# Performance work log

Hardware: AMD Instinct MI355X
Metric: run time of the kernel (lower is better)

The kernel has to match this reference:

```python
import jax, jax.numpy as jnp
import numpy as np
from jax import lax

WS = 7          # window size
SHIFT = WS // 2 # shift for odd blocks
NH = 4          # num heads
PATCH = 4


def _rel_index(ws):
    # standard Swin relative position index, shape (ws*ws, ws*ws)
    coords = np.stack(np.meshgrid(np.arange(ws), np.arange(ws), indexing='ij')).reshape(2, -1)
    rel = (coords[:, :, None] - coords[:, None, :]).transpose(1, 2, 0)
    rel[..., 0] += ws - 1
    rel[..., 1] += ws - 1
    rel[..., 0] *= 2 * ws - 1
    return jnp.asarray(rel.sum(-1))


def _attn_mask(H, W, ws, s):
    # BasicLayer mask for cyclic shift: (nW, ws*ws, ws*ws) with 0 / -100
    img = np.zeros((H, W))
    cnt = 0
    for hs in (slice(0, -ws), slice(-ws, -s), slice(-s, None)):
        for wsl in (slice(0, -ws), slice(-ws, -s), slice(-s, None)):
            img[hs, wsl] = cnt
            cnt += 1
    mw = img.reshape(H // ws, ws, W // ws, ws).transpose(0, 2, 1, 3).reshape(-1, ws * ws)
    diff = mw[:, None, :] - mw[:, :, None]
    return jnp.asarray(np.where(diff != 0, -100.0, 0.0).astype(np.float32))


def setup_inputs() -> dict:
    key = jax.random.key(0)
    ks = jax.random.split(key, 6)
    C = 128
    return {
        'x': jax.random.normal(ks[0], (16, 3, 448, 448), jnp.float32),
        'conv_w': jax.random.normal(ks[1], (C, 3, PATCH, PATCH), jnp.float32) * 0.02,
        'conv_b': jnp.zeros((C,), jnp.float32),
        'qkv_w': jax.random.normal(ks[2], (2, 3 * C, C), jnp.float32) * 0.02,
        'qkv_b': jnp.zeros((2, 3 * C), jnp.float32),
        'proj_w': jax.random.normal(ks[3], (2, C, C), jnp.float32) * 0.02,
        'proj_b': jnp.zeros((2, C), jnp.float32),
        'rpb': jax.random.normal(ks[4], (2, (2 * WS - 1) ** 2, NH), jnp.float32) * 0.02,
    }


def _forward(x, conv_w, conv_b, qkv_w, qkv_b, proj_w, proj_b, rpb):
    # patch embed: strided conv
    y = lax.conv_general_dilated(x, conv_w, (PATCH, PATCH), 'VALID',
                                 dimension_numbers=('NCHW', 'OIHW', 'NCHW'))
    y = y + conv_b[None, :, None, None]
    B, C, H, W = y.shape
    hd = C // NH
    scale = hd ** -0.5
    N = WS * WS
    nW = (H // WS) * (W // WS)
    t = y.reshape(B, C, H * W).transpose(0, 2, 1)  # (B, L, C)

    rel_idx = _rel_index(WS)                    # (N, N)
    mask = _attn_mask(H, W, WS, SHIFT)          # (nW, N, N)

    for i in range(2):
        shift = 0 if i % 2 == 0 else SHIFT
        xw = t.reshape(B, H, W, C)
        if shift > 0:
            xw = jnp.roll(xw, (-shift, -shift), axis=(1, 2))
        # window partition -> (B*nW, N, C)
        win = xw.reshape(B, H // WS, WS, W // WS, WS, C).transpose(0, 1, 3, 2, 4, 5).reshape(-1, N, C)
        qkv = win @ qkv_w[i].T + qkv_b[i]       # (B*nW, N, 3C)
        qkv = qkv.reshape(-1, N, 3, NH, hd).transpose(2, 0, 3, 1, 4)
        q, k, v = qkv[0], qkv[1], qkv[2]        # (B*nW, NH, N, hd)
        attn = jnp.einsum('wnid,wnjd->wnij', q * scale, k)
        bias = rpb[i][rel_idx].transpose(2, 0, 1)  # (NH, N, N)
        attn = attn + bias[None]
        if shift > 0:
            attn = (attn.reshape(B, nW, NH, N, N) + mask[None, :, None]).reshape(-1, NH, N, N)
        attn = jax.nn.softmax(attn, axis=-1)
        out = jnp.einsum('wnij,wnjd->wnid', attn, v).transpose(0, 2, 1, 3).reshape(-1, N, C)
        out = out @ proj_w[i].T + proj_b[i]
        # window reverse
        xw = out.reshape(B, H // WS, W // WS, WS, WS, C).transpose(0, 1, 3, 2, 4, 5).reshape(B, H, W, C)
        if shift > 0:
            xw = jnp.roll(xw, (shift, shift), axis=(1, 2))
        t = xw.reshape(B, H * W, C)

    return t.reshape(B, H, W, C).transpose(0, 3, 1, 2)  # (B, C, H, W)


def reference(x, conv_w, conv_b, qkv_w, qkv_b, proj_w, proj_b, rpb):
    return _forward(x, conv_w, conv_b, qkv_w, qkv_b, proj_w, proj_b, rpb)
```

## Files before the change

kernel.cpp:

```cpp
#include <hip/hip_runtime.h>

#define BB 16
#define CC 128
#define HH 112
#define NHH 4
#define WSZ 7
#define NN 49
#define SH 3

typedef _Float16 h8 __attribute__((ext_vector_type(8)));
typedef _Float16 h4 __attribute__((ext_vector_type(4)));
typedef float f4 __attribute__((ext_vector_type(4)));

__device__ __forceinline__ int rid3(int p) { return p < 105 ? 0 : (p < 109 ? 1 : 2); }

#define OFF_WIN 0
#define OFF_K   8704
#define OFF_Q   18944
#define OFF_VT  29184
#define OFF_P   0
#define OFF_O   18944

__global__ __launch_bounds__(256) void conv_embed(const float* __restrict__ x,
    const float* __restrict__ cw, const float* __restrict__ cb, _Float16* __restrict__ t0) {
  __shared__ float xs[3][4][448];
  __shared__ float wT[48][128];
  __shared__ float cbs[128];
  int bid = blockIdx.x;
  int b = bid / HH, oh = bid % HH;
  int tid = threadIdx.x;
  for (int idx = tid; idx < 3 * 4 * 448; idx += 256) {
    int ch = idx / 1792;
    int r = (idx / 448) & 3;
    int col = idx % 448;
    xs[ch][r][col] = x[((b * 3 + ch) * 448 + (oh * 4 + r)) * 448 + col];
  }
  for (int idx = tid; idx < 6144; idx += 256) {
    int c = idx / 48, k = idx - c * 48;
    wT[k][c] = cw[idx];
  }
  if (tid < 128) cbs[tid] = cb[tid];
  __syncthreads();
  int c0 = (tid & 31) << 2;
  int gg = tid >> 5;
  for (int it = 0; it < 4; ++it) {
    int gw0 = it * 32 + gg * 4;
    if (gw0 >= HH) break;
    float acc[4][4] = {};
#pragma unroll
    for (int k = 0; k < 48; ++k) {
      int ch = k >> 4, r = (k >> 2) & 3, j = k & 3;
      float4 wv = *(const float4*)&wT[k][c0];
#pragma unroll
      for (int d = 0; d < 4; ++d) {
        float xv = xs[ch][r][(gw0 + d) * 4 + j];
        acc[d][0] = fmaf(xv, wv.x, acc[d][0]);
        acc[d][1] = fmaf(xv, wv.y, acc[d][1]);
        acc[d][2] = fmaf(xv, wv.z, acc[d][2]);
        acc[d][3] = fmaf(xv, wv.w, acc[d][3]);
      }
    }
    float4 bv = *(const float4*)&cbs[c0];
#pragma unroll
    for (int d = 0; d < 4; ++d) {
      int gw = gw0 + d;
      h4 o;
      o[0] = (_Float16)(acc[d][0] + bv.x); o[1] = (_Float16)(acc[d][1] + bv.y);
      o[2] = (_Float16)(acc[d][2] + bv.z); o[3] = (_Float16)(acc[d][3] + bv.w);
      *(h4*)&t0[((size_t)(b * HH + oh) * HH + gw) * CC + c0] = o;
    }
  }
}

__global__ void prep(const float* __restrict__ qw, const float* __restrict__ qb,
                     const float* __restrict__ pw, const float* __restrict__ rpb,
                     _Float16* __restrict__ qwh, float* __restrict__ qbs,
                     _Float16* __restrict__ pwh, float* __restrict__ biasT) {
  const float scale = 0.17677669529663687f;
  int tid0 = blockIdx.x * blockDim.x + threadIdx.x;
  int stride = gridDim.x * blockDim.x;
  for (int idx = tid0; idx < 2 * 384 * 128; idx += stride) {
    int n = (idx >> 7) % 384;
    float v = qw[idx];
    if (n < 128) v *= scale;
    qwh[idx] = (_Float16)v;
  }
  for (int idx = tid0; idx < 2 * 384; idx += stride) {
    int n = idx % 384;
    float v = qb[idx];
    if (n < 128) v *= scale;
    qbs[idx] = v;
  }
  for (int idx = tid0; idx < 2 * 128 * 128; idx += stride)
    pwh[idx] = (_Float16)pw[idx];
  for (int idx = tid0; idx < 2 * 4 * 4 * 4 * 64 * 4; idx += stride) {
    int r = idx & 3;
    int lane = (idx >> 2) & 63;
    int it = (idx >> 8) & 3;
    int jt = (idx >> 10) & 3;
    int hh = (idx >> 12) & 3;
    int ll = idx >> 14;
    int i = it * 16 + (lane & 15);
    int j = jt * 16 + ((lane >> 4) * 4) + r;
    float v = 0.f;
    if (i < NN && j < NN) {
      int rel = ((i / 7 - j / 7) + 6) * 13 + ((i % 7 - j % 7) + 6);
      v = rpb[(ll * 169 + rel) * NHH + hh];
    }
    biasT[idx] = v;
  }
}

__global__ __launch_bounds__(256, 2) void swin_layer(
    const _Float16* __restrict__ tin, _Float16* __restrict__ toutB, float* __restrict__ outN,
    const _Float16* __restrict__ qwh, const float* __restrict__ qbs,
    const _Float16* __restrict__ pwh, const float* __restrict__ pb,
    const float* __restrict__ biasT, int shift, int writeN) {
  __shared__ _Float16 sm[38400];

  int tid = threadIdx.x;
  int wid = blockIdx.x;
  int b = wid >> 8;
  int wh = (wid >> 4) & 15, ww = wid & 15;
  int w = tid >> 6, l = tid & 63;
  int li = l & 15, lg = l >> 4;

  for (int c = tid; c < 64 * 16; c += 256) {
    int n = c >> 4, k0 = (c & 15) * 8;
    h8 v = {0, 0, 0, 0, 0, 0, 0, 0};
    if (n < NN) {
      int gh = wh * WSZ + n / 7 + shift; if (gh >= HH) gh -= HH;
      int gw = ww * WSZ + n % 7 + shift; if (gw >= HH) gw -= HH;
      v = *(const h8*)(tin + ((size_t)(b * HH + gh) * HH + gw) * CC + k0);
    }
    *(h8*)&sm[OFF_WIN + n * 136 + k0] = v;
  }
  __syncthreads();

  {
    h8 bW[4][4];
#pragma unroll
    for (int nt = 0; nt < 4; ++nt)
#pragma unroll
      for (int ks = 0; ks < 4; ++ks)
        bW[nt][ks] = *(const h8*)&sm[OFF_WIN + (nt * 16 + li) * 136 + ks * 32 + lg * 8];
    for (int mi = 0; mi < 6; ++mi) {
      int mt = w * 6 + mi;
      const _Float16* arow = qwh + (size_t)(mt * 16 + li) * 128 + lg * 8;
      h8 aA[4];
#pragma unroll
      for (int ks = 0; ks < 4; ++ks) aA[ks] = *(const h8*)(arow + ks * 32);
      f4 acc[4] = {};
#pragma unroll
      for (int ks = 0; ks < 4; ++ks)
#pragma unroll
        for (int nt = 0; nt < 4; ++nt)
          acc[nt] = __builtin_amdgcn_mfma_f32_16x16x32_f16(aA[ks], bW[nt][ks], acc[nt], 0, 0, 0);
      int dbase = mt * 16 + lg * 4;
      float4 bb = *(const float4*)&qbs[dbase];
#pragma unroll
      for (int nt = 0; nt < 4; ++nt) {
        int i = nt * 16 + li;
        float v0 = acc[nt][0] + bb.x, v1 = acc[nt][1] + bb.y;
        float v2 = acc[nt][2] + bb.z, v3 = acc[nt][3] + bb.w;
        if (mt < 8) {
          int hq = dbase >> 5, dh = dbase & 31;
          h4 v = {(_Float16)v0, (_Float16)v1, (_Float16)v2, (_Float16)v3};
          *(h4*)&sm[OFF_Q + hq * 2560 + i * 40 + dh] = v;
        } else if (mt < 16) {
          int d = dbase - 128, hq = d >> 5, dh = d & 31;
          h4 v = {(_Float16)v0, (_Float16)v1, (_Float16)v2, (_Float16)v3};
          *(h4*)&sm[OFF_K + hq * 2560 + i * 40 + dh] = v;
        } else {
          int d = dbase - 256, hq = d >> 5, dh = d & 31;
          sm[OFF_VT + hq * 2304 + (dh + 0) * 72 + i] = (_Float16)v0;
          sm[OFF_VT + hq * 2304 + (dh + 1) * 72 + i] = (_Float16)v1;
          sm[OFF_VT + hq * 2304 + (dh + 2) * 72 + i] = (_Float16)v2;
          sm[OFF_VT + hq * 2304 + (dh + 3) * 72 + i] = (_Float16)v3;
        }
      }
    }
  }
  __syncthreads();

  float inv[4];
  {
    int h = w;
    h8 aK[4], bQ[4];
#pragma unroll
    for (int jt = 0; jt < 4; ++jt)
      aK[jt] = *(const h8*)&sm[OFF_K + h * 2560 + (jt * 16 + li) * 40 + lg * 8];
#pragma unroll
    for (int it = 0; it < 4; ++it)
      bQ[it] = *(const h8*)&sm[OFF_Q + h * 2560 + (it * 16 + li) * 40 + lg * 8];
    f4 s[4][4] = {};
#pragma unroll
    for (int jt = 0; jt < 4; ++jt)
#pragma unroll
      for (int it = 0; it < 4; ++it)
        s[jt][it] = __builtin_amdgcn_mfma_f32_16x16x32_f16(aK[jt], bQ[it], s[jt][it], 0, 0, 0);
    const float* bT = biasT + h * 4096;
#pragma unroll
    for (int jt = 0; jt < 4; ++jt)
#pragma unroll
      for (int it = 0; it < 4; ++it) {
        f4 bb = *(const f4*)&bT[(jt * 4 + it) * 256 + l * 4];
#pragma unroll
        for (int r = 0; r < 4; ++r) {
          int j = jt * 16 + lg * 4 + r;
          float v = s[jt][it][r] + bb[r];
          s[jt][it][r] = (j < NN) ? v : -1e30f;
        }
      }
    if (shift && (wh == 15 || ww == 15)) {
      int regi[4], regj[4][4];
#pragma unroll
      for (int it = 0; it < 4; ++it) {
        int i = it * 16 + li;
        regi[it] = rid3(wh * WSZ + i / 7) * 3 + rid3(ww * WSZ + i % 7);
      }
#pragma unroll
      for (int jt = 0; jt < 4; ++jt)
#pragma unroll
        for (int r = 0; r < 4; ++r) {
          int j = jt * 16 + lg * 4 + r;
          regj[jt][r] = rid3(wh * WSZ + j / 7) * 3 + rid3(ww * WSZ + j % 7);
        }
#pragma unroll
      for (int jt = 0; jt < 4; ++jt)
#pragma unroll
        for (int it = 0; it < 4; ++it)
#pragma unroll
          for (int r = 0; r < 4; ++r)
            if (regj[jt][r] != regi[it]) s[jt][it][r] -= 100.f;
    }
    __syncthreads();

#pragma unroll
    for (int it = 0; it < 4; ++it) {
      float mx = -1e30f;
#pragma unroll
      for (int jt = 0; jt < 4; ++jt)
#pragma unroll
        for (int r = 0; r < 4; ++r) mx = fmaxf(mx, s[jt][it][r]);
      mx = fmaxf(mx, __shfl_xor(mx, 16));
      mx = fmaxf(mx, __shfl_xor(mx, 32));
      float sum = 0.f;
#pragma unroll
      for (int jt = 0; jt < 4; ++jt)
#pragma unroll
        for (int r = 0; r < 4; ++r) {
          float e = __expf(s[jt][it][r] - mx);
          s[jt][it][r] = e;
          sum += e;
        }
      sum += __shfl_xor(sum, 16);
      sum += __shfl_xor(sum, 32);
      inv[it] = 1.f / sum;
    }
#pragma unroll
    for (int it = 0; it < 4; ++it)
#pragma unroll
      for (int jt = 0; jt < 4; ++jt) {
        int i = it * 16 + li, j0 = jt * 16 + lg * 4;
        h4 v = {(_Float16)s[jt][it][0], (_Float16)s[jt][it][1],
                (_Float16)s[jt][it][2], (_Float16)s[jt][it][3]};
        *(h4*)&sm[OFF_P + h * 4608 + i * 72 + j0] = v;
      }
  }

  {
    int h = w;
    h8 aV[2][2], bP[4][2];
#pragma unroll
    for (int mt = 0; mt < 2; ++mt)
#pragma unroll
      for (int ks = 0; ks < 2; ++ks)
        aV[mt][ks] = *(const h8*)&sm[OFF_VT + h * 2304 + (mt * 16 + li) * 72 + ks * 32 + lg * 8];
#pragma unroll
    for (int nt = 0; nt < 4; ++nt)
#pragma unroll
      for (int ks = 0; ks < 2; ++ks)
        bP[nt][ks] = *(const h8*)&sm[OFF_P + h * 4608 + (nt * 16 + li) * 72 + ks * 32 + lg * 8];
    f4 o[2][4] = {};
#pragma unroll
    for (int ks = 0; ks < 2; ++ks)
#pragma unroll
      for (int mt = 0; mt < 2; ++mt)
#pragma unroll
        for (int nt = 0; nt < 4; ++nt)
          o[mt][nt] = __builtin_amdgcn_mfma_f32_16x16x32_f16(aV[mt][ks], bP[nt][ks], o[mt][nt], 0, 0, 0);
#pragma unroll
    for (int mt = 0; mt < 2; ++mt)
#pragma unroll
      for (int nt = 0; nt < 4; ++nt) {
        int i = nt * 16 + li;
        int d = h * 32 + mt * 16 + lg * 4;
        float is = inv[nt];
        h4 v = {(_Float16)(o[mt][nt][0] * is), (_Float16)(o[mt][nt][1] * is),
                (_Float16)(o[mt][nt][2] * is), (_Float16)(o[mt][nt][3] * is)};
        *(h4*)&sm[OFF_O + i * 136 + d] = v;
      }
  }
  __syncthreads();

  {
    h8 bO[4][4];
#pragma unroll
    for (int nt = 0; nt < 4; ++nt)
#pragma unroll
      for (int ks = 0; ks < 4; ++ks)
        bO[nt][ks] = *(const h8*)&sm[OFF_O + (nt * 16 + li) * 136 + ks * 32 + lg * 8];
    for (int mi = 0; mi < 2; ++mi) {
      int mt = w * 2 + mi;
      const _Float16* arow = pwh + (size_t)(mt * 16 + li) * 128 + lg * 8;
      h8 aP[4];
#pragma unroll
      for (int ks = 0; ks < 4; ++ks) aP[ks] = *(const h8*)(arow + ks * 32);
      f4 acc[4] = {};
#pragma unroll
      for (int ks = 0; ks < 4; ++ks)
#pragma unroll
        for (int nt = 0; nt < 4; ++nt)
          acc[nt] = __builtin_amdgcn_mfma_f32_16x16x32_f16(aP[ks], bO[nt][ks], acc[nt], 0, 0, 0);
      int dbase = mt * 16 + lg * 4;
      float4 bb = *(const float4*)&pb[dbase];
#pragma unroll
      for (int nt = 0; nt < 4; ++nt) {
        int i = nt * 16 + li;
        if (i < NN) {
          int gh = wh * WSZ + i / 7 + shift; if (gh >= HH) gh -= HH;
          int gw = ww * WSZ + i % 7 + shift; if (gw >= HH) gw -= HH;
          float v0 = acc[nt][0] + bb.x, v1 = acc[nt][1] + bb.y;
          float v2 = acc[nt][2] + bb.z, v3 = acc[nt][3] + bb.w;
          if (!writeN) {
            h4 v = {(_Float16)v0, (_Float16)v1, (_Float16)v2, (_Float16)v3};
            *(h4*)&toutB[((size_t)(b * HH + gh) * HH + gw) * CC + dbase] = v;
          } else {
            size_t base = ((size_t)(b * CC + dbase) * HH + gh) * HH + gw;
            outN[base] = v0;
            outN[base + (size_t)HH * HH] = v1;
            outN[base + (size_t)2 * HH * HH] = v2;
            outN[base + (size_t)3 * HH * HH] = v3;
          }
        }
      }
    }
  }
}

extern "C" void kernel_launch(void* const* d_in, const int* in_sizes, int n_in,
                              void* d_out, int out_size, void* d_ws, size_t ws_size,
                              hipStream_t stream) {
  const float* x = (const float*)d_in[0];
  const float* cw = (const float*)d_in[1];
  const float* cb = (const float*)d_in[2];
  const float* qkvw = (const float*)d_in[3];
  const float* qkvb = (const float*)d_in[4];
  const float* projw = (const float*)d_in[5];
  const float* projb = (const float*)d_in[6];
  const float* rpb = (const float*)d_in[7];
  float* out = (float*)d_out;

  char* ws = (char*)d_ws;
  _Float16* t0 = (_Float16*)ws;
  size_t off = (size_t)BB * HH * HH * CC * 2;
  _Float16* qwh = (_Float16*)(ws + off);  off += 2 * 384 * 128 * 2;
  _Float16* pwh = (_Float16*)(ws + off);  off += 2 * 128 * 128 * 2;
  float* qbs = (float*)(ws + off);        off += 2 * 384 * 4;
  float* biasT = (float*)(ws + off);

  prep<<<224, 256, 0, stream>>>(qkvw, qkvb, projw, rpb, qwh, qbs, pwh, biasT);
  conv_embed<<<BB * HH, 256, 0, stream>>>(x, cw, cb, t0);

  swin_layer<<<4096, 256, 0, stream>>>(t0, t0, nullptr,
      qwh, qbs, pwh, projb, biasT, 0, 0);
  swin_layer<<<4096, 256, 0, stream>>>(t0, nullptr, out,
      qwh + 384 * 128, qbs + 384, pwh + 128 * 128, projb + 128,
      biasT + 16384, SH, 1);
}
```

Before: 317.1 us.

## Cut swin_layer LDS with swizzled layouts and direct-global window loads

Window tokens for the QKV GEMM are now loaded straight from global memory into registers instead of being staged in LDS. Q/K/V/P/O tiles use an XOR-swizzled unpadded layout, which shrinks LDS from about 77KB to 49KB and allows occupancy to rise from 2 to 3 blocks per CU. Unshifted fp16 outputs are staged through LDS so the global write is coalesced 16-byte rows. In exchange there are extra barriers, a larger accumulator register footprint that may pressure the occupancy target, and redundant global reads of the QKV weights inside the k-loop.

```diff
diff --git a/kernel.cpp b/kernel.cpp
--- a/kernel.cpp
+++ b/kernel.cpp
@@ -14,12 +14,14 @@
 
 __device__ __forceinline__ int rid3(int p) { return p < 105 ? 0 : (p < 109 ? 1 : 2); }
 
-#define OFF_WIN 0
-#define OFF_K   8704
-#define OFF_Q   18944
-#define OFF_VT  29184
-#define OFF_P   0
-#define OFF_O   18944
+#define SWZ(row, j, CH) ((row) * ((CH) * 8) + (((((j) >> 3) ^ (row)) & ((CH) - 1)) << 3) + ((j) & 7))
+
+#define KB 0
+#define QB 8192
+#define VB 16384
+#define PB 0
+#define OB 16384
+#define YB 0
 
 __global__ __launch_bounds__(256) void conv_embed(const float* __restrict__ x,
     const float* __restrict__ cw, const float* __restrict__ cb, _Float16* __restrict__ t0) {
@@ -111,12 +113,12 @@
   }
 }
 
-__global__ __launch_bounds__(256, 2) void swin_layer(
+__global__ __launch_bounds__(256, 3) void swin_layer(
     const _Float16* __restrict__ tin, _Float16* __restrict__ toutB, float* __restrict__ outN,
     const _Float16* __restrict__ qwh, const float* __restrict__ qbs,
     const _Float16* __restrict__ pwh, const float* __restrict__ pb,
     const float* __restrict__ biasT, int shift, int writeN) {
-  __shared__ _Float16 sm[38400];
+  __shared__ _Float16 sm[24576];
 
   int tid = threadIdx.x;
   int wid = blockIdx.x;
@@ -125,58 +127,56 @@
   int w = tid >> 6, l = tid & 63;
   int li = l & 15, lg = l >> 4;
 
-  for (int c = tid; c < 64 * 16; c += 256) {
-    int n = c >> 4, k0 = (c & 15) * 8;
-    h8 v = {0, 0, 0, 0, 0, 0, 0, 0};
-    if (n < NN) {
-      int gh = wh * WSZ + n / 7 + shift; if (gh >= HH) gh -= HH;
-      int gw = ww * WSZ + n % 7 + shift; if (gw >= HH) gw -= HH;
-      v = *(const h8*)(tin + ((size_t)(b * HH + gh) * HH + gw) * CC + k0);
-    }
-    *(h8*)&sm[OFF_WIN + n * 136 + k0] = v;
-  }
-  __syncthreads();
+  const _Float16* tokp[4];
+#pragma unroll
+  for (int nt = 0; nt < 4; ++nt) {
+    int n = nt * 16 + li;
+    int gh = wh * WSZ + n / 7 + shift; if (gh >= HH) gh -= HH;
+    int gw = ww * WSZ + n % 7 + shift; if (gw >= HH) gw -= HH;
+    tokp[nt] = tin + ((size_t)(b * HH + gh) * HH + gw) * CC;
+  }
 
   {
-    h8 bW[4][4];
-#pragma unroll
-    for (int nt = 0; nt < 4; ++nt)
-#pragma unroll
-      for (int ks = 0; ks < 4; ++ks)
-        bW[nt][ks] = *(const h8*)&sm[OFF_WIN + (nt * 16 + li) * 136 + ks * 32 + lg * 8];
+    f4 acc[6][4] = {};
+#pragma unroll
+    for (int ks = 0; ks < 4; ++ks) {
+      h8 bW[4];
+#pragma unroll
+      for (int nt = 0; nt < 4; ++nt)
+        bW[nt] = *(const h8*)(tokp[nt] + ks * 32 + lg * 8);
+#pragma unroll
+      for (int mi = 0; mi < 6; ++mi) {
+        int mt = w * 6 + mi;
+        h8 a = *(const h8*)(qwh + (size_t)(mt * 16 + li) * 128 + ks * 32 + lg * 8);
+#pragma unroll
+        for (int nt = 0; nt < 4; ++nt)
+          acc[mi][nt] = __builtin_amdgcn_mfma_f32_16x16x32_f16(a, bW[nt], acc[mi][nt], 0, 0, 0);
+      }
+    }
+#pragma unroll
     for (int mi = 0; mi < 6; ++mi) {
       int mt = w * 6 + mi;
-      const _Float16* arow = qwh + (size_t)(mt * 16 + li) * 128 + lg * 8;
-      h8 aA[4];
-#pragma unroll
-      for (int ks = 0; ks < 4; ++ks) aA[ks] = *(const h8*)(arow + ks * 32);
-      f4 acc[4] = {};
-#pragma unroll
-      for (int ks = 0; ks < 4; ++ks)
-#pragma unroll
-        for (int nt = 0; nt < 4; ++nt)
-          acc[nt] = __builtin_amdgcn_mfma_f32_16x16x32_f16(aA[ks], bW[nt][ks], acc[nt], 0, 0, 0);
       int dbase = mt * 16 + lg * 4;
       float4 bb = *(const float4*)&qbs[dbase];
 #pragma unroll
       for (int nt = 0; nt < 4; ++nt) {
         int i = nt * 16 + li;
-        float v0 = acc[nt][0] + bb.x, v1 = acc[nt][1] + bb.y;
-        float v2 = acc[nt][2] + bb.z, v3 = acc[nt][3] + bb.w;
+        float v0 = acc[mi][nt][0] + bb.x, v1 = acc[mi][nt][1] + bb.y;
+        float v2 = acc[mi][nt][2] + bb.z, v3 = acc[mi][nt][3] + bb.w;
         if (mt < 8) {
           int hq = dbase >> 5, dh = dbase & 31;
           h4 v = {(_Float16)v0, (_Float16)v1, (_Float16)v2, (_Float16)v3};
-          *(h4*)&sm[OFF_Q + hq * 2560 + i * 40 + dh] = v;
+          *(h4*)&sm[QB + hq * 2048 + SWZ(i, dh, 4)] = v;
         } else if (mt < 16) {
           int d = dbase - 128, hq = d >> 5, dh = d & 31;
           h4 v = {(_Float16)v0, (_Float16)v1, (_Float16)v2, (_Float16)v3};
-          *(h4*)&sm[OFF_K + hq * 2560 + i * 40 + dh] = v;
+          *(h4*)&sm[KB + hq * 2048 + SWZ(i, dh, 4)] = v;
         } else {
           int d = dbase - 256, hq = d >> 5, dh = d & 31;
-          sm[OFF_VT + hq * 2304 + (dh + 0) * 72 + i] = (_Float16)v0;
-          sm[OFF_VT + hq * 2304 + (dh + 1) * 72 + i] = (_Float16)v1;
-          sm[OFF_VT + hq * 2304 + (dh + 2) * 72 + i] = (_Float16)v2;
-          sm[OFF_VT + hq * 2304 + (dh + 3) * 72 + i] = (_Float16)v3;
+          sm[VB + hq * 2048 + SWZ(dh + 0, i, 8)] = (_Float16)v0;
+          sm[VB + hq * 2048 + SWZ(dh + 1, i, 8)] = (_Float16)v1;
+          sm[VB + hq * 2048 + SWZ(dh + 2, i, 8)] = (_Float16)v2;
+          sm[VB + hq * 2048 + SWZ(dh + 3, i, 8)] = (_Float16)v3;
         }
       }
     }
@@ -189,10 +189,10 @@
     h8 aK[4], bQ[4];
 #pragma unroll
     for (int jt = 0; jt < 4; ++jt)
-      aK[jt] = *(const h8*)&sm[OFF_K + h * 2560 + (jt * 16 + li) * 40 + lg * 8];
+      aK[jt] = *(const h8*)&sm[KB + h * 2048 + SWZ(jt * 16 + li, lg * 8, 4)];
 #pragma unroll
     for (int it = 0; it < 4; ++it)
-      bQ[it] = *(const h8*)&sm[OFF_Q + h * 2560 + (it * 16 + li) * 40 + lg * 8];
+      bQ[it] = *(const h8*)&sm[QB + h * 2048 + SWZ(it * 16 + li, lg * 8, 4)];
     f4 s[4][4] = {};
 #pragma unroll
     for (int jt = 0; jt < 4; ++jt)
@@ -265,7 +265,7 @@
         int i = it * 16 + li, j0 = jt * 16 + lg * 4;
         h4 v = {(_Float16)s[jt][it][0], (_Float16)s[jt][it][1],
                 (_Float16)s[jt][it][2], (_Float16)s[jt][it][3]};
-        *(h4*)&sm[OFF_P + h * 4608 + i * 72 + j0] = v;
+        *(h4*)&sm[PB + h * 4096 + SWZ(i, j0, 8)] = v;
       }
   }
 
@@ -276,12 +276,12 @@
     for (int mt = 0; mt < 2; ++mt)
 #pragma unroll
       for (int ks = 0; ks < 2; ++ks)
-        aV[mt][ks] = *(const h8*)&sm[OFF_VT + h * 2304 + (mt * 16 + li) * 72 + ks * 32 + lg * 8];
+        aV[mt][ks] = *(const h8*)&sm[VB + h * 2048 + SWZ(mt * 16 + li, ks * 32 + lg * 8, 8)];
 #pragma unroll
     for (int nt = 0; nt < 4; ++nt)
 #pragma unroll
       for (int ks = 0; ks < 2; ++ks)
-        bP[nt][ks] = *(const h8*)&sm[OFF_P + h * 4608 + (nt * 16 + li) * 72 + ks * 32 + lg * 8];
+        bP[nt][ks] = *(const h8*)&sm[PB + h * 4096 + SWZ(nt * 16 + li, ks * 32 + lg * 8, 8)];
     f4 o[2][4] = {};
 #pragma unroll
     for (int ks = 0; ks < 2; ++ks)
@@ -290,6 +290,7 @@
 #pragma unroll
         for (int nt = 0; nt < 4; ++nt)
           o[mt][nt] = __builtin_amdgcn_mfma_f32_16x16x32_f16(aV[mt][ks], bP[nt][ks], o[mt][nt], 0, 0, 0);
+    __syncthreads();
 #pragma unroll
     for (int mt = 0; mt < 2; ++mt)
 #pragma unroll
@@ -299,49 +300,65 @@
         float is = inv[nt];
         h4 v = {(_Float16)(o[mt][nt][0] * is), (_Float16)(o[mt][nt][1] * is),
                 (_Float16)(o[mt][nt][2] * is), (_Float16)(o[mt][nt][3] * is)};
-        *(h4*)&sm[OFF_O + i * 136 + d] = v;
+        *(h4*)&sm[OB + SWZ(i, d, 16)] = v;
       }
   }
   __syncthreads();
 
   {
-    h8 bO[4][4];
-#pragma unroll
-    for (int nt = 0; nt < 4; ++nt)
-#pragma unroll
-      for (int ks = 0; ks < 4; ++ks)
-        bO[nt][ks] = *(const h8*)&sm[OFF_O + (nt * 16 + li) * 136 + ks * 32 + lg * 8];
-    for (int mi = 0; mi < 2; ++mi) {
-      int mt = w * 2 + mi;
-      const _Float16* arow = pwh + (size_t)(mt * 16 + li) * 128 + lg * 8;
-      h8 aP[4];
-#pragma unroll
-      for (int ks = 0; ks < 4; ++ks) aP[ks] = *(const h8*)(arow + ks * 32);
-      f4 acc[4] = {};
-#pragma unroll
-      for (int ks = 0; ks < 4; ++ks)
+    f4 acc[2][4] = {};
+#pragma unroll
+    for (int ks = 0; ks < 4; ++ks) {
+      h8 bO[4];
+#pragma unroll
+      for (int nt = 0; nt < 4; ++nt)
+        bO[nt] = *(const h8*)&sm[OB + SWZ(nt * 16 + li, ks * 32 + lg * 8, 16)];
+#pragma unroll
+      for (int mi = 0; mi < 2; ++mi) {
+        int mt = w * 2 + mi;
+        h8 a = *(const h8*)(pwh + (size_t)(mt * 16 + li) * 128 + ks * 32 + lg * 8);
 #pragma unroll
         for (int nt = 0; nt < 4; ++nt)
-          acc[nt] = __builtin_amdgcn_mfma_f32_16x16x32_f16(aP[ks], bO[nt][ks], acc[nt], 0, 0, 0);
-      int dbase = mt * 16 + lg * 4;
-      float4 bb = *(const float4*)&pb[dbase];
-#pragma unroll
-      for (int nt = 0; nt < 4; ++nt) {
-        int i = nt * 16 + li;
-        if (i < NN) {
-          int gh = wh * WSZ + i / 7 + shift; if (gh >= HH) gh -= HH;
-          int gw = ww * WSZ + i % 7 + shift; if (gw >= HH) gw -= HH;
-          float v0 = acc[nt][0] + bb.x, v1 = acc[nt][1] + bb.y;
-          float v2 = acc[nt][2] + bb.z, v3 = acc[nt][3] + bb.w;
-          if (!writeN) {
-            h4 v = {(_Float16)v0, (_Float16)v1, (_Float16)v2, (_Float16)v3};
-            *(h4*)&toutB[((size_t)(b * HH + gh) * HH + gw) * CC + dbase] = v;
-          } else {
+          acc[mi][nt] = __builtin_amdgcn_mfma_f32_16x16x32_f16(a, bO[nt], acc[mi][nt], 0, 0, 0);
+      }
+    }
+    if (!writeN) {
+#pragma unroll
+      for (int mi = 0; mi < 2; ++mi) {
+        int dbase = (w * 2 + mi) * 16 + lg * 4;
+        float4 bb = *(const float4*)&pb[dbase];
+#pragma unroll
+        for (int nt = 0; nt < 4; ++nt) {
+          int i = nt * 16 + li;
+          h4 v = {(_Float16)(acc[mi][nt][0] + bb.x), (_Float16)(acc[mi][nt][1] + bb.y),
+                  (_Float16)(acc[mi][nt][2] + bb.z), (_Float16)(acc[mi][nt][3] + bb.w)};
+          *(h4*)&sm[YB + SWZ(i, dbase, 16)] = v;
+        }
+      }
+      __syncthreads();
+      for (int cidx = tid; cidx < NN * 16; cidx += 256) {
+        int tok = cidx >> 4, c = cidx & 15;
+        h8 v = *(const h8*)&sm[YB + SWZ(tok, c * 8, 16)];
+        int gh = wh * WSZ + tok / 7;
+        int gw = ww * WSZ + tok % 7;
+        *(h8*)&toutB[((size_t)(b * HH + gh) * HH + gw) * CC + c * 8] = v;
+      }
+    } else {
+#pragma unroll
+      for (int mi = 0; mi < 2; ++mi) {
+        int dbase = (w * 2 + mi) * 16 + lg * 4;
+        float4 bb = *(const float4*)&pb[dbase];
+#pragma unroll
+        for (int nt = 0; nt < 4; ++nt) {
+          int i = nt * 16 + li;
+          if (i < NN) {
+            int gh = wh * WSZ + i / 7 + shift; if (gh >= HH) gh -= HH;
+            int gw = ww * WSZ + i % 7 + shift; if (gw >= HH) gw -= HH;
             size_t base = ((size_t)(b * CC + dbase) * HH + gh) * HH + gw;
-            outN[base] = v0;
-            outN[base + (size_t)HH * HH] = v1;
-            outN[base + (size_t)2 * HH * HH] = v2;
-            outN[base + (size_t)3 * HH * HH] = v3;
+            outN[base] = acc[mi][nt][0] + bb.x;
+            outN[base + (size_t)HH * HH] = acc[mi][nt][1] + bb.y;
+            outN[base + (size_t)2 * HH * HH] = acc[mi][nt][2] + bb.z;
+            outN[base + (size_t)3 * HH * HH] = acc[mi][nt][3] + bb.w;
           }
         }
       }
```

Result: slower. 377.0 us (+18.9%).
